# Kernel optimization log

Hardware: AMD Instinct MI355X
Metric: run time of the kernel (lower is better)

The kernel has to match this reference:

```python
import jax, jax.numpy as jnp
import numpy as np

BN_EPS = 1e-5


def _guide_net(fullres, w1, b1, bn_gamma, bn_beta, bn_mean, bn_var, w2, b2):
    # two 1x1 convs == channel matmuls
    x = jnp.einsum('nchw,oc->nohw', fullres, w1[:, :, 0, 0]) + b1[None, :, None, None]
    inv = bn_gamma / jnp.sqrt(bn_var + BN_EPS)
    x = (x - bn_mean[None, :, None, None]) * inv[None, :, None, None] + bn_beta[None, :, None, None]
    x = jax.nn.relu(x)
    g = jnp.einsum('nchw,oc->nohw', x, w2[:, :, 0, 0]) + b2[None, :, None, None]
    return jax.nn.sigmoid(g)  # [N,1,H,W] in (0,1)


def _slice_one(grid_n, guide_n):
    # grid_n: [C,D,h,w]; guide_n: [H,W]; trilinear grid_sample, align_corners=True.
    C, D, h, w = grid_n.shape
    H, W = guide_n.shape
    # normalized coords in torch code map exactly to voxel coords [0, size-1]
    gz = guide_n * (D - 1)                      # per-pixel depth coord [H,W]
    z0f = jnp.floor(gz)
    tz = (gz - z0f)[None, :, :]                 # [1,H,W]
    z0 = jnp.clip(z0f, 0, D - 1).astype(jnp.int32)
    z1 = jnp.clip(z0f + 1, 0, D - 1).astype(jnp.int32)
    gy = jnp.linspace(0.0, h - 1.0, H)
    y0f = jnp.floor(gy)
    ty = (gy - y0f)[None, :, None]              # [1,H,1]
    y0 = jnp.clip(y0f, 0, h - 1).astype(jnp.int32)[:, None]
    y1 = jnp.clip(y0f + 1, 0, h - 1).astype(jnp.int32)[:, None]
    gx = jnp.linspace(0.0, w - 1.0, W)
    x0f = jnp.floor(gx)
    tx = (gx - x0f)[None, None, :]              # [1,1,W]
    x0 = jnp.clip(x0f, 0, w - 1).astype(jnp.int32)[None, :]
    x1 = jnp.clip(x0f + 1, 0, w - 1).astype(jnp.int32)[None, :]

    def g(z, y, x):
        # z:[H,W], y:[H,1], x:[1,W] -> broadcast gather -> [C,H,W]
        return grid_n[:, z, y, x]

    def lerp_xy(z):
        a = g(z, y0, x0) * (1 - tx) + g(z, y0, x1) * tx
        b = g(z, y1, x0) * (1 - tx) + g(z, y1, x1) * tx
        return a * (1 - ty) + b * ty

    return lerp_xy(z0) * (1 - tz) + lerp_xy(z1) * tz  # [C,H,W]


def _apply_coeffs(coeff, fullres):
    # coeff: [N,12,H,W]; rows (0:3,+3), (4:7,+7), (8:11,+11)
    N, _, H, W = coeff.shape
    A = coeff[:, jnp.array([0, 1, 2, 4, 5, 6, 8, 9, 10])].reshape(N, 3, 3, H, W)
    bias = coeff[:, jnp.array([3, 7, 11])]
    return jnp.einsum('nkchw,nchw->nkhw', A, fullres) + bias


def setup_inputs() -> dict:
    key = jax.random.key(0)
    ks = jax.random.split(key, 10)
    N, H, W = 2, 1080, 1920
    return {
        'fullres': jax.random.uniform(ks[0], (N, 3, H, W), jnp.float32),
        'bilateral_grid': jax.random.normal(ks[1], (N, 12, 8, 16, 16), jnp.float32),
        'w1': jax.random.normal(ks[2], (16, 3, 1, 1), jnp.float32) * 0.2,
        'b1': jax.random.normal(ks[3], (16,), jnp.float32) * 0.1,
        'bn_gamma': jax.random.uniform(ks[4], (16,), jnp.float32, 0.5, 1.5),
        'bn_beta': jax.random.normal(ks[5], (16,), jnp.float32) * 0.1,
        'bn_mean': jax.random.normal(ks[6], (16,), jnp.float32) * 0.1,
        'bn_var': jax.random.uniform(ks[7], (16,), jnp.float32, 0.5, 1.5),
        'w2': jax.random.normal(ks[8], (1, 16, 1, 1), jnp.float32) * 0.2,
        'b2': jax.random.normal(ks[9], (1,), jnp.float32) * 0.1,
    }


def reference(fullres, bilateral_grid, w1, b1, bn_gamma, bn_beta, bn_mean, bn_var, w2, b2):
    guide = _guide_net(fullres, w1, b1, bn_gamma, bn_beta, bn_mean, bn_var, w2, b2)  # [N,1,H,W]
    coeff = jax.vmap(_slice_one)(bilateral_grid, guide[:, 0])                         # [N,12,H,W]
    return _apply_coeffs(coeff, fullres)                                              # [N,3,H,W]
```

## Files before the change

### kernel.cpp

```cpp
#include <hip/hip_runtime.h>
#include <hip/hip_bf16.h>
#include <math.h>

#define HWV (1080 * 1920)

typedef _Float16 half2 __attribute__((ext_vector_type(2)));
typedef __fp16   pk2   __attribute__((ext_vector_type(2)));
union U32H2 { unsigned u; half2 h; pk2 p; };

__global__ void prep_w(const float* __restrict__ w1, const float* __restrict__ b1,
                       const float* __restrict__ gamma, const float* __restrict__ beta,
                       const float* __restrict__ mean, const float* __restrict__ var,
                       const float* __restrict__ w2, const float* __restrict__ b2,
                       float* __restrict__ wsw) {
    int i = threadIdx.x;
    if (i < 16) {
        float inv = gamma[i] / sqrtf(var[i] + 1e-5f);
        float wr = w1[i*3+0] * inv, wg = w1[i*3+1] * inv, wb = w1[i*3+2] * inv;
        float bs = (b1[i] - mean[i]) * inv + beta[i];
        wsw[64 + i] = w2[i];
        unsigned* wp = (unsigned*)(wsw + 84);
        U32H2 t;
        t.p = __builtin_amdgcn_cvt_pkrtz(wr, wr); wp[i*4+0] = t.u;
        t.p = __builtin_amdgcn_cvt_pkrtz(wg, wg); wp[i*4+1] = t.u;
        t.p = __builtin_amdgcn_cvt_pkrtz(wb, wb); wp[i*4+2] = t.u;
        t.p = __builtin_amdgcn_cvt_pkrtz(bs, bs); wp[i*4+3] = t.u;
    }
    if (i == 0) wsw[80] = b2[0];
}

__global__ __launch_bounds__(512, 8) void fused_kernel(
        const float* __restrict__ fullres,
        const float* __restrict__ grid,
        const float* __restrict__ wsw,
        float* __restrict__ out) {
    __shared__ unsigned slo[9][9][4];
    __shared__ unsigned shi[9][9][2];

    const int tid = threadIdx.x;
    const int n   = blockIdx.z;
    const int y   = blockIdx.y;
    const int xs  = blockIdx.x * 1024;
    const int x   = xs + 2 * tid;
    const bool act = (x < 1920);

    const int p = y * 1920 + min(x, 1918);
    const float* fr = fullres + n * 3 * HWV + p;
    float2 R = *(const float2*)(fr);
    float2 G = *(const float2*)(fr + HWV);
    float2 B = *(const float2*)(fr + 2 * HWV);

    const int a = (int)((float)xs * (15.0f / 1919.0f));
    {
        float gy = (float)y * (15.0f / 1079.0f);
        float y0f = floorf(gy);
        float ty = gy - y0f;
        int y0 = min((int)y0f, 15);
        int y1 = min(y0 + 1, 15);
        const int dy = (y1 - y0) * 16;
        const float* gb = grid + n * 24576 + y0 * 16;
        if (tid < 486) {
            int j   = tid / 81;
            int rem = tid - j * 81;
            int z   = rem / 9;
            int k   = rem - z * 9;
            int zz  = min(z, 7);
            int xc  = min(a + k, 15);
            const float* q0 = gb + (2 * j) * 2048 + zz * 256 + xc;
            const float* q1 = q0 + 2048;
            float v00 = q0[0], v01 = q0[dy];
            float v10 = q1[0], v11 = q1[dy];
            float e0 = fmaf(ty, v01 - v00, v00);
            float e1 = fmaf(ty, v11 - v10, v10);
            U32H2 t;
            t.p = __builtin_amdgcn_cvt_pkrtz(e0, e1);
            if (j < 4) slo[k][z][j] = t.u;
            else       shi[k][z][j - 4] = t.u;
        }
    }
    __syncthreads();

    if (!act) return;

    U32H2 rr, gg, bb;
    rr.p = __builtin_amdgcn_cvt_pkrtz(R.x, R.y);
    gg.p = __builtin_amdgcn_cvt_pkrtz(G.x, G.y);
    bb.p = __builtin_amdgcn_cvt_pkrtz(B.x, B.y);
    const unsigned* wp = (const unsigned*)(wsw + 84);
    const half2 zero = {(_Float16)0.0f, (_Float16)0.0f};
    float b2s = wsw[80];
    float acc0 = b2s, acc1 = b2s;
#pragma unroll
    for (int c = 0; c < 16; ++c) {
        U32H2 wr, wg, wb, bs;
        wr.u = wp[4*c+0]; wg.u = wp[4*c+1]; wb.u = wp[4*c+2]; bs.u = wp[4*c+3];
        half2 h = wr.h * rr.h + (wg.h * gg.h + (wb.h * bb.h + bs.h));
        h = __builtin_elementwise_max(h, zero);
        float w2c = wsw[64 + c];
        acc0 = fmaf((float)h.x, w2c, acc0);
        acc1 = fmaf((float)h.y, w2c, acc1);
    }

    float accv[2] = {acc0, acc1};
    float rv[2] = {R.x, R.y}, gv[2] = {G.x, G.y}, bv[2] = {B.x, B.y};
    float outr[2], outg[2], outb[2];

#pragma unroll
    for (int q = 0; q < 2; ++q) {
        float e = __expf(-accv[q]);
        float guide = __builtin_amdgcn_rcpf(1.0f + e);
        float gz = guide * 7.0f;
        float z0f = floorf(gz);
        float tz = gz - z0f;
        int z0 = min((int)z0f, 7);
        int z1 = z0 + 1;

        float gx = (float)(x + q) * (15.0f / 1919.0f);
        float x0f = floorf(gx);
        float tx = gx - x0f;
        int x0 = (int)x0f;
        int k0 = x0 - a;
        int k1 = min(x0 + 1, 15) - a;

        float wx0 = 1.0f - tx, wx1 = tx;
        float wz0 = 1.0f - tz, wz1 = tz;

        U32H2 w00h, w01h, w10h, w11h;
        w00h.p = __builtin_amdgcn_cvt_pkrtz(wx0 * wz0, wx0 * wz0);
        w01h.p = __builtin_amdgcn_cvt_pkrtz(wx0 * wz1, wx0 * wz1);
        w10h.p = __builtin_amdgcn_cvt_pkrtz(wx1 * wz0, wx1 * wz0);
        w11h.p = __builtin_amdgcn_cvt_pkrtz(wx1 * wz1, wx1 * wz1);

        const uint4 A0 = *(const uint4*)&slo[k0][z0][0];
        const uint4 A1 = *(const uint4*)&slo[k0][z1][0];
        const uint4 B0 = *(const uint4*)&slo[k1][z0][0];
        const uint4 B1 = *(const uint4*)&slo[k1][z1][0];
        const uint2 C0 = *(const uint2*)&shi[k0][z0][0];
        const uint2 C1 = *(const uint2*)&shi[k0][z1][0];
        const uint2 D0 = *(const uint2*)&shi[k1][z0][0];
        const uint2 D1 = *(const uint2*)&shi[k1][z1][0];

        unsigned a0j[6] = {A0.x, A0.y, A0.z, A0.w, C0.x, C0.y};
        unsigned a1j[6] = {A1.x, A1.y, A1.z, A1.w, C1.x, C1.y};
        unsigned b0j[6] = {B0.x, B0.y, B0.z, B0.w, D0.x, D0.y};
        unsigned b1j[6] = {B1.x, B1.y, B1.z, B1.w, D1.x, D1.y};

        half2 hc[6];
#pragma unroll
        for (int j = 0; j < 6; ++j) {
            U32H2 ua0, ua1, ub0, ub1;
            ua0.u = a0j[j]; ua1.u = a1j[j]; ub0.u = b0j[j]; ub1.u = b1j[j];
            half2 h = w00h.h * ua0.h + (w01h.h * ua1.h);
            h = w10h.h * ub0.h + h;
            h = w11h.h * ub1.h + h;
            hc[j] = h;
        }

        outr[q] = fmaf((float)hc[0].x, rv[q], fmaf((float)hc[0].y, gv[q],
                  fmaf((float)hc[1].x, bv[q], (float)hc[1].y)));
        outg[q] = fmaf((float)hc[2].x, rv[q], fmaf((float)hc[2].y, gv[q],
                  fmaf((float)hc[3].x, bv[q], (float)hc[3].y)));
        outb[q] = fmaf((float)hc[4].x, rv[q], fmaf((float)hc[4].y, gv[q],
                  fmaf((float)hc[5].x, bv[q], (float)hc[5].y)));
    }

    float* op = out + n * 3 * HWV + p;
    *(float2*)(op)           = make_float2(outr[0], outr[1]);
    *(float2*)(op + HWV)     = make_float2(outg[0], outg[1]);
    *(float2*)(op + 2 * HWV) = make_float2(outb[0], outb[1]);
}

extern "C" void kernel_launch(void* const* d_in, const int* in_sizes, int n_in,
                              void* d_out, int out_size, void* d_ws, size_t ws_size,
                              hipStream_t stream) {
    const float* fullres = (const float*)d_in[0];
    const float* grid    = (const float*)d_in[1];
    const float* w1      = (const float*)d_in[2];
    const float* b1      = (const float*)d_in[3];
    const float* gamma   = (const float*)d_in[4];
    const float* beta    = (const float*)d_in[5];
    const float* mean    = (const float*)d_in[6];
    const float* var     = (const float*)d_in[7];
    const float* w2      = (const float*)d_in[8];
    const float* b2      = (const float*)d_in[9];
    float* out = (float*)d_out;

    float* wsw = (float*)d_ws;

    prep_w<<<1, 64, 0, stream>>>(w1, b1, gamma, beta, mean, var, w2, b2, wsw);

    dim3 grid_dim(2, 1080, 2);
    fused_kernel<<<grid_dim, 512, 0, stream>>>(fullres, grid, wsw, out);
}
```

Before: 32.25 us.

## Precompute per-column x weights, accumulate guide in fp16, reorder grid dims

Moves the per-column x interpolation indices and fp16 weights into a lookup table built by the prep kernel, so the main kernel loads them instead of recomputing floor and conversions. The second guide-net convolution now accumulates in packed fp16 instead of fp32 FMAs. Weight products are formed in half precision, and the launch grid is reordered so the two batch images for the same row sit in adjacent blocks. Doing the accumulation and weight products in fp16 reduces accuracy of the guide and the interpolation weights, which could shift the depth index near bin boundaries.

```diff
diff --git a/kernel.cpp b/kernel.cpp
--- a/kernel.cpp
+++ b/kernel.cpp
@@ -13,20 +13,37 @@
                        const float* __restrict__ mean, const float* __restrict__ var,
                        const float* __restrict__ w2, const float* __restrict__ b2,
                        float* __restrict__ wsw) {
-    int i = threadIdx.x;
+    int i = blockIdx.x * blockDim.x + threadIdx.x;
+    unsigned* wp = (unsigned*)(wsw + 84);
     if (i < 16) {
         float inv = gamma[i] / sqrtf(var[i] + 1e-5f);
         float wr = w1[i*3+0] * inv, wg = w1[i*3+1] * inv, wb = w1[i*3+2] * inv;
         float bs = (b1[i] - mean[i]) * inv + beta[i];
-        wsw[64 + i] = w2[i];
-        unsigned* wp = (unsigned*)(wsw + 84);
         U32H2 t;
         t.p = __builtin_amdgcn_cvt_pkrtz(wr, wr); wp[i*4+0] = t.u;
         t.p = __builtin_amdgcn_cvt_pkrtz(wg, wg); wp[i*4+1] = t.u;
         t.p = __builtin_amdgcn_cvt_pkrtz(wb, wb); wp[i*4+2] = t.u;
         t.p = __builtin_amdgcn_cvt_pkrtz(bs, bs); wp[i*4+3] = t.u;
-    }
-    if (i == 0) wsw[80] = b2[0];
+        float w2c = w2[i];
+        t.p = __builtin_amdgcn_cvt_pkrtz(w2c, w2c); wp[64 + i] = t.u;
+    }
+    if (i == 16) {
+        float b2s = b2[0];
+        U32H2 t;
+        t.p = __builtin_amdgcn_cvt_pkrtz(b2s, b2s); wp[80] = t.u;
+    }
+    if (i < 1920) {
+        float gx = (float)i * (15.0f / 1919.0f);
+        float x0f = floorf(gx);
+        float tx = gx - x0f;
+        int x0 = (int)x0f;
+        int x1 = min(x0 + 1, 15);
+        U32H2 a0, a1;
+        a0.p = __builtin_amdgcn_cvt_pkrtz(1.0f - tx, 1.0f - tx);
+        a1.p = __builtin_amdgcn_cvt_pkrtz(tx, tx);
+        uint4* colinfo = (uint4*)(wsw + 168);
+        colinfo[i] = make_uint4((unsigned)(x0 | (x1 << 8)), a0.u, a1.u, 0u);
+    }
 }
 
 __global__ __launch_bounds__(512, 8) void fused_kernel(
@@ -38,45 +55,47 @@
     __shared__ unsigned shi[9][9][2];
 
     const int tid = threadIdx.x;
-    const int n   = blockIdx.z;
-    const int y   = blockIdx.y;
-    const int xs  = blockIdx.x * 1024;
+    const int seg = blockIdx.x;
+    const int n   = blockIdx.y;
+    const int y   = blockIdx.z;
+    const int xs  = seg * 1024;
     const int x   = xs + 2 * tid;
     const bool act = (x < 1920);
-
-    const int p = y * 1920 + min(x, 1918);
+    const int a = (int)((float)xs * (15.0f / 1919.0f));
+    const int pcol = min(x, 1918);
+    const int p = y * 1920 + pcol;
+
     const float* fr = fullres + n * 3 * HWV + p;
     float2 R = *(const float2*)(fr);
     float2 G = *(const float2*)(fr + HWV);
     float2 B = *(const float2*)(fr + 2 * HWV);
-
-    const int a = (int)((float)xs * (15.0f / 1919.0f));
-    {
+    const uint4* colinfo = (const uint4*)(wsw + 168);
+    uint4 ci0 = colinfo[pcol];
+    uint4 ci1 = colinfo[pcol + 1];
+
+    if (tid < 486) {
         float gy = (float)y * (15.0f / 1079.0f);
         float y0f = floorf(gy);
         float ty = gy - y0f;
         int y0 = min((int)y0f, 15);
         int y1 = min(y0 + 1, 15);
         const int dy = (y1 - y0) * 16;
-        const float* gb = grid + n * 24576 + y0 * 16;
-        if (tid < 486) {
-            int j   = tid / 81;
-            int rem = tid - j * 81;
-            int z   = rem / 9;
-            int k   = rem - z * 9;
-            int zz  = min(z, 7);
-            int xc  = min(a + k, 15);
-            const float* q0 = gb + (2 * j) * 2048 + zz * 256 + xc;
-            const float* q1 = q0 + 2048;
-            float v00 = q0[0], v01 = q0[dy];
-            float v10 = q1[0], v11 = q1[dy];
-            float e0 = fmaf(ty, v01 - v00, v00);
-            float e1 = fmaf(ty, v11 - v10, v10);
-            U32H2 t;
-            t.p = __builtin_amdgcn_cvt_pkrtz(e0, e1);
-            if (j < 4) slo[k][z][j] = t.u;
-            else       shi[k][z][j - 4] = t.u;
-        }
+        int j   = tid / 81;
+        int rem = tid - j * 81;
+        int z   = rem / 9;
+        int k   = rem - z * 9;
+        int zz  = min(z, 7);
+        int xc  = min(a + k, 15);
+        const float* q0 = grid + n * 24576 + (2 * j) * 2048 + zz * 256 + y0 * 16 + xc;
+        const float* q1 = q0 + 2048;
+        float v00 = q0[0], v01 = q0[dy];
+        float v10 = q1[0], v11 = q1[dy];
+        float e0 = fmaf(ty, v01 - v00, v00);
+        float e1 = fmaf(ty, v11 - v10, v10);
+        U32H2 t;
+        t.p = __builtin_amdgcn_cvt_pkrtz(e0, e1);
+        if (j < 4) slo[k][z][j] = t.u;
+        else       shi[k][z][j - 4] = t.u;
     }
     __syncthreads();
 
@@ -88,22 +107,21 @@
     bb.p = __builtin_amdgcn_cvt_pkrtz(B.x, B.y);
     const unsigned* wp = (const unsigned*)(wsw + 84);
     const half2 zero = {(_Float16)0.0f, (_Float16)0.0f};
-    float b2s = wsw[80];
-    float acc0 = b2s, acc1 = b2s;
+    U32H2 accp; accp.u = wp[80];
 #pragma unroll
     for (int c = 0; c < 16; ++c) {
-        U32H2 wr, wg, wb, bs;
+        U32H2 wr, wg, wb, bs, w2d;
         wr.u = wp[4*c+0]; wg.u = wp[4*c+1]; wb.u = wp[4*c+2]; bs.u = wp[4*c+3];
+        w2d.u = wp[64 + c];
         half2 h = wr.h * rr.h + (wg.h * gg.h + (wb.h * bb.h + bs.h));
         h = __builtin_elementwise_max(h, zero);
-        float w2c = wsw[64 + c];
-        acc0 = fmaf((float)h.x, w2c, acc0);
-        acc1 = fmaf((float)h.y, w2c, acc1);
-    }
-
-    float accv[2] = {acc0, acc1};
+        accp.h = h * w2d.h + accp.h;
+    }
+    float accv[2] = {(float)accp.h.x, (float)accp.h.y};
+
     float rv[2] = {R.x, R.y}, gv[2] = {G.x, G.y}, bv[2] = {B.x, B.y};
     float outr[2], outg[2], outb[2];
+    uint4 civ[2] = {ci0, ci1};
 
 #pragma unroll
     for (int q = 0; q < 2; ++q) {
@@ -115,21 +133,20 @@
         int z0 = min((int)z0f, 7);
         int z1 = z0 + 1;
 
-        float gx = (float)(x + q) * (15.0f / 1919.0f);
-        float x0f = floorf(gx);
-        float tx = gx - x0f;
-        int x0 = (int)x0f;
-        int k0 = x0 - a;
-        int k1 = min(x0 + 1, 15) - a;
-
-        float wx0 = 1.0f - tx, wx1 = tx;
-        float wz0 = 1.0f - tz, wz1 = tz;
-
-        U32H2 w00h, w01h, w10h, w11h;
-        w00h.p = __builtin_amdgcn_cvt_pkrtz(wx0 * wz0, wx0 * wz0);
-        w01h.p = __builtin_amdgcn_cvt_pkrtz(wx0 * wz1, wx0 * wz1);
-        w10h.p = __builtin_amdgcn_cvt_pkrtz(wx1 * wz0, wx1 * wz0);
-        w11h.p = __builtin_amdgcn_cvt_pkrtz(wx1 * wz1, wx1 * wz1);
+        int k0 = (int)(civ[q].x & 255u) - a;
+        int k1 = (int)((civ[q].x >> 8) & 255u) - a;
+        U32H2 wx0d, wx1d;
+        wx0d.u = civ[q].y;
+        wx1d.u = civ[q].z;
+
+        U32H2 wz0d, wz1d;
+        wz0d.p = __builtin_amdgcn_cvt_pkrtz(1.0f - tz, 1.0f - tz);
+        wz1d.p = __builtin_amdgcn_cvt_pkrtz(tz, tz);
+
+        half2 w00 = wx0d.h * wz0d.h;
+        half2 w01 = wx0d.h * wz1d.h;
+        half2 w10 = wx1d.h * wz0d.h;
+        half2 w11 = wx1d.h * wz1d.h;
 
         const uint4 A0 = *(const uint4*)&slo[k0][z0][0];
         const uint4 A1 = *(const uint4*)&slo[k0][z1][0];
@@ -150,9 +167,9 @@
         for (int j = 0; j < 6; ++j) {
             U32H2 ua0, ua1, ub0, ub1;
             ua0.u = a0j[j]; ua1.u = a1j[j]; ub0.u = b0j[j]; ub1.u = b1j[j];
-            half2 h = w00h.h * ua0.h + (w01h.h * ua1.h);
-            h = w10h.h * ub0.h + h;
-            h = w11h.h * ub1.h + h;
+            half2 h = w00 * ua0.h + (w01 * ua1.h);
+            h = w10 * ub0.h + h;
+            h = w11 * ub1.h + h;
             hc[j] = h;
         }
 
@@ -187,8 +204,8 @@
 
     float* wsw = (float*)d_ws;
 
-    prep_w<<<1, 64, 0, stream>>>(w1, b1, gamma, beta, mean, var, w2, b2, wsw);
-
-    dim3 grid_dim(2, 1080, 2);
+    prep_w<<<8, 256, 0, stream>>>(w1, b1, gamma, beta, mean, var, w2, b2, wsw);
+
+    dim3 grid_dim(2, 2, 1080);
     fused_kernel<<<grid_dim, 512, 0, stream>>>(fullres, grid, wsw, out);
 }
```

After: 31.00 us, median of 2. -3.9%, faster.
